# Optimization experiments

Hardware: AMD Instinct MI355X
Metric: run time of the kernel (lower is better)

## Reference

```python
import jax, jax.numpy as jnp
import numpy as np

B, P, L = 1024, 8, 16384  # batch, PRECISION_BITS, TRNG_BITSTREAM_LENGTH


def setup_inputs() -> dict:
    key = jax.random.key(0)
    k1, k2 = jax.random.split(key)
    num = jax.random.randint(k1, (B,), 0, 2 ** P, dtype=jnp.int32)
    # per-module TRNG bitstreams, length P + L (as in Module.__init__)
    r = jax.random.randint(k2, (B, P, P + L), 0, 2, dtype=jnp.int32)
    return {"num": num, "r": r}


def reference(num, r):
    # Module index i reads x[P-1-i] of the MSB-first binary string -> bit i (LSB-first)
    Bsz, Pb, T = r.shape
    Lb = T - Pb
    x = ((num[:, None] >> jnp.arange(Pb, dtype=num.dtype)) & 1).astype(r.dtype)  # [B,P]
    rt = jnp.moveaxis(r, -1, 0)  # [T,B,P]

    def step(y, r_c):
        # majority scheme: y_o = x&y | x&r | y&r  (vectorized over batch and modules)
        y_o = (x & y) | (x & r_c) | (y & r_c)
        # pipeline: y_i[i, t+1] = y_o[i-1, t]; module 0 keeps y_i = 0 forever
        y_next = jnp.concatenate([jnp.zeros((Bsz, 1), r.dtype), y_o[:, :-1]], axis=1)
        return y_next, y_o[:, -1]  # snarf last module's output

    _, outs = jax.lax.scan(step, jnp.zeros((Bsz, Pb), r.dtype), rt)  # outs: [T,B]
    # sn[cyc] = y_o[P-1] from cycle cyc-1; first P entries are invalid and trimmed
    sn = outs[Pb - 1 : Pb - 1 + Lb].T  # [B, L]
    return sn
```

## Files before the change

### kernel.cpp

```cpp
#include <hip/hip_runtime.h>


#define BATCH 1024
#define PBITS 8
#define LBITS 16384
#define TLEN (PBITS + LBITS)

#define CHUNK 4096
#define STAGE_DW 4104

typedef const __attribute__((address_space(1))) void gvoid;
typedef __attribute__((address_space(3))) void lvoid;

__global__ __launch_bounds__(256) void sng_kernel(const int* __restrict__ num,
                                                  const int* __restrict__ r,
                                                  int* __restrict__ out) {
    __shared__ int lds[STAGE_DW];

    const int t = threadIdx.x;
    const int b = blockIdx.x >> 2;
    const int jb = (blockIdx.x & 3) << 12;

    const int nb = num[b];
    const int* rowbase = r + (size_t)b * (PBITS * TLEN) + jb;

    int v[16];
#pragma unroll
    for (int k = 0; k < 16; ++k) v[k] = 0;

#pragma unroll
    for (int i = 0; i < PBITS; ++i) {
        const int* src = rowbase + i * TLEN;
#pragma unroll
        for (int k = 0; k < 4; ++k)
            __builtin_amdgcn_global_load_lds((gvoid*)(src + 4 * (t + 256 * k)),
                                             (lvoid*)(&lds[4 * (t + 256 * k)]),
                                             16, 0, 0);
        if (t < 2)
            __builtin_amdgcn_global_load_lds((gvoid*)(src + 4 * (1024 + t)),
                                             (lvoid*)(&lds[4 * (1024 + t)]),
                                             16, 0, 0);
        __syncthreads();

        const int* lp = &lds[t + i];
        if ((nb >> i) & 1) {
#pragma unroll
            for (int k = 0; k < 16; ++k) v[k] |= lp[256 * k];
        } else {
#pragma unroll
            for (int k = 0; k < 16; ++k) v[k] &= lp[256 * k];
        }
        __syncthreads();
    }

    int* ob = out + (size_t)b * LBITS + jb + t;
#pragma unroll
    for (int k = 0; k < 16; ++k)
        __builtin_nontemporal_store(v[k], ob + 256 * k);
}

extern "C" void kernel_launch(void* const* d_in, const int* in_sizes, int n_in,
                              void* d_out, int out_size, void* d_ws, size_t ws_size,
                              hipStream_t stream) {
    const int* num = (const int*)d_in[0];
    const int* r   = (const int*)d_in[1];
    int* out = (int*)d_out;

    const int blocks = BATCH * 4;
    sng_kernel<<<blocks, 256, 0, stream>>>(num, r, out);
}
```

Measured before the change: 699.2 us.

## Replace LDS staging with direct vector loads and skip leading zero-bit rows

Removes the LDS staging buffer and its two barriers per bit row. Each thread now owns 16 consecutive outputs, reads a 20-int window with five 16-byte nontemporal loads, and writes its results with vector stores. Rows below the lowest set bit of num are skipped, since AND-ing a zero accumulator leaves it zero. In exchange each thread loads 25% more data per row through overlapping windows, and register pressure rises.

```diff
diff --git a/kernel.cpp b/kernel.cpp
--- a/kernel.cpp
+++ b/kernel.cpp
@@ -6,23 +6,20 @@
 #define LBITS 16384
 #define TLEN (PBITS + LBITS)
 
-#define CHUNK 4096
-#define STAGE_DW 4104
-
-typedef const __attribute__((address_space(1))) void gvoid;
-typedef __attribute__((address_space(3))) void lvoid;
+typedef int v4i __attribute__((ext_vector_type(4)));
 
 __global__ __launch_bounds__(256) void sng_kernel(const int* __restrict__ num,
                                                   const int* __restrict__ r,
                                                   int* __restrict__ out) {
-    __shared__ int lds[STAGE_DW];
-
     const int t = threadIdx.x;
     const int b = blockIdx.x >> 2;
     const int jb = (blockIdx.x & 3) << 12;
+    const int l = jb + (t << 4);
 
     const int nb = num[b];
-    const int* rowbase = r + (size_t)b * (PBITS * TLEN) + jb;
+    const int start = __builtin_ctz(nb | (1 << PBITS));
+
+    const int* rb = r + (size_t)b * (PBITS * TLEN) + l;
 
     int v[16];
 #pragma unroll
@@ -30,33 +27,34 @@
 
 #pragma unroll
     for (int i = 0; i < PBITS; ++i) {
-        const int* src = rowbase + i * TLEN;
+        if (i < start) continue;
+        const int* p = rb + (size_t)i * TLEN + 4 * (i >> 2);
+        int a[20];
 #pragma unroll
-        for (int k = 0; k < 4; ++k)
-            __builtin_amdgcn_global_load_lds((gvoid*)(src + 4 * (t + 256 * k)),
-                                             (lvoid*)(&lds[4 * (t + 256 * k)]),
-                                             16, 0, 0);
-        if (t < 2)
-            __builtin_amdgcn_global_load_lds((gvoid*)(src + 4 * (1024 + t)),
-                                             (lvoid*)(&lds[4 * (1024 + t)]),
-                                             16, 0, 0);
-        __syncthreads();
-
-        const int* lp = &lds[t + i];
+        for (int q = 0; q < 5; ++q) {
+            const v4i w = __builtin_nontemporal_load(
+                reinterpret_cast<const v4i*>(p + 4 * q));
+            a[4 * q + 0] = w.x; a[4 * q + 1] = w.y;
+            a[4 * q + 2] = w.z; a[4 * q + 3] = w.w;
+        }
+        const int s = i & 3;
         if ((nb >> i) & 1) {
 #pragma unroll
-            for (int k = 0; k < 16; ++k) v[k] |= lp[256 * k];
+            for (int k = 0; k < 16; ++k) v[k] |= a[s + k];
         } else {
 #pragma unroll
-            for (int k = 0; k < 16; ++k) v[k] &= lp[256 * k];
+            for (int k = 0; k < 16; ++k) v[k] &= a[s + k];
         }
-        __syncthreads();
     }
 
-    int* ob = out + (size_t)b * LBITS + jb + t;
+    int* o = out + (size_t)b * LBITS + l;
 #pragma unroll
-    for (int k = 0; k < 16; ++k)
-        __builtin_nontemporal_store(v[k], ob + 256 * k);
+    for (int q = 0; q < 4; ++q) {
+        v4i w;
+        w.x = v[4 * q + 0]; w.y = v[4 * q + 1];
+        w.z = v[4 * q + 2]; w.w = v[4 * q + 3];
+        __builtin_nontemporal_store(w, reinterpret_cast<v4i*>(o + 4 * q));
+    }
 }
 
 extern "C" void kernel_launch(void* const* d_in, const int* in_sizes, int n_in,
```

New measurement: 754.3 us. 7.9% more time.

## Issue all row loads up front, skip rows below lowest set bit

Applied to the files above, without the earlier changes.

Each block now handles a 1024-element chunk instead of 4096, giving four times as many blocks. It issues the global-to-LDS loads for all needed rows at once into six separate LDS buffers, with a single barrier instead of two barriers per row. Rows 0 and 4 are aligned, so they are loaded straight into registers with nontemporal loads. Rows below the lowest set bit of num are skipped, because an AND into an all-zero accumulator leaves it zero. The aim is more memory parallelism and fewer serialized load/sync phases, at the cost of more LDS per block and more blocks.

```diff
diff --git a/kernel.cpp b/kernel.cpp
--- a/kernel.cpp
+++ b/kernel.cpp
@@ -6,57 +6,82 @@
 #define LBITS 16384
 #define TLEN (PBITS + LBITS)
 
-#define CHUNK 4096
-#define STAGE_DW 4104
-
 typedef const __attribute__((address_space(1))) void gvoid;
 typedef __attribute__((address_space(3))) void lvoid;
 
-__global__ __launch_bounds__(256) void sng_kernel(const int* __restrict__ num,
-                                                  const int* __restrict__ r,
-                                                  int* __restrict__ out) {
-    __shared__ int lds[STAGE_DW];
+__global__ __launch_bounds__(256, 4) void sng_kernel(const int* __restrict__ num,
+                                                     const int* __restrict__ r,
+                                                     int* __restrict__ out) {
+    __shared__ int lds[6][1032];
 
     const int t = threadIdx.x;
-    const int b = blockIdx.x >> 2;
-    const int jb = (blockIdx.x & 3) << 12;
+    const int b = blockIdx.x >> 4;
+    const int jb = (blockIdx.x & 15) << 10;
 
     const int nb = num[b];
-    const int* rowbase = r + (size_t)b * (PBITS * TLEN) + jb;
+    const int start = __builtin_ctz(nb | 256);
 
-    int v[16];
-#pragma unroll
-    for (int k = 0; k < 16; ++k) v[k] = 0;
+    const int* rb = r + (size_t)b * (PBITS * TLEN) + jb;
 
 #pragma unroll
     for (int i = 0; i < PBITS; ++i) {
-        const int* src = rowbase + i * TLEN;
+        if ((i & 3) == 0) continue;
+        if (i >= start) {
+            const int si = (i < 4) ? (i - 1) : (i - 2);
+            const int* src = rb + (size_t)i * TLEN;
+            __builtin_amdgcn_global_load_lds((gvoid*)(src + 4 * t),
+                                             (lvoid*)(&lds[si][4 * t]), 16, 0, 0);
+            if (t < 2)
+                __builtin_amdgcn_global_load_lds((gvoid*)(src + 1024 + 4 * t),
+                                                 (lvoid*)(&lds[si][1024 + 4 * t]),
+                                                 16, 0, 0);
+        }
+    }
+
+    int d0[4], d4[4];
+    if (start == 0) {
 #pragma unroll
         for (int k = 0; k < 4; ++k)
-            __builtin_amdgcn_global_load_lds((gvoid*)(src + 4 * (t + 256 * k)),
-                                             (lvoid*)(&lds[4 * (t + 256 * k)]),
-                                             16, 0, 0);
-        if (t < 2)
-            __builtin_amdgcn_global_load_lds((gvoid*)(src + 4 * (1024 + t)),
-                                             (lvoid*)(&lds[4 * (1024 + t)]),
-                                             16, 0, 0);
-        __syncthreads();
+            d0[k] = __builtin_nontemporal_load(rb + t + 256 * k);
+    }
+    if (start <= 4) {
+#pragma unroll
+        for (int k = 0; k < 4; ++k)
+            d4[k] = __builtin_nontemporal_load(rb + (size_t)4 * TLEN + 4 + t + 256 * k);
+    }
 
-        const int* lp = &lds[t + i];
+    __syncthreads();
+
+    int v[4] = {0, 0, 0, 0};
+#pragma unroll
+    for (int i = 0; i < PBITS; ++i) {
+        if (i < start) continue;
+        int a[4];
+        if (i == 0) {
+#pragma unroll
+            for (int k = 0; k < 4; ++k) a[k] = d0[k];
+        } else if (i == 4) {
+#pragma unroll
+            for (int k = 0; k < 4; ++k) a[k] = d4[k];
+        } else {
+            const int si = (i < 4) ? (i - 1) : (i - 2);
+#pragma unroll
+            for (int k = 0; k < 4; ++k)
+                a[k] = lds[si][t + i + 256 * k];
+        }
         if ((nb >> i) & 1) {
 #pragma unroll
-            for (int k = 0; k < 16; ++k) v[k] |= lp[256 * k];
+            for (int k = 0; k < 4; ++k) v[k] |= a[k];
         } else {
 #pragma unroll
-            for (int k = 0; k < 16; ++k) v[k] &= lp[256 * k];
+            for (int k = 0; k < 4; ++k) v[k] &= a[k];
         }
-        __syncthreads();
     }
 
-    int* ob = out + (size_t)b * LBITS + jb + t;
+    int* o = out + (size_t)b * LBITS + jb + t;
 #pragma unroll
-    for (int k = 0; k < 16; ++k)
-        __builtin_nontemporal_store(v[k], ob + 256 * k);
+    for (int k = 0; k < 4; ++k)
+        __builtin_nontemporal_store(v[k], o + 256 * k);
 }
 
 extern "C" void kernel_launch(void* const* d_in, const int* in_sizes, int n_in,
@@ -66,6 +91,6 @@
     const int* r   = (const int*)d_in[1];
     int* out = (int*)d_out;
 
-    const int blocks = BATCH * 4;
+    const int blocks = BATCH * 16;
     sng_kernel<<<blocks, 256, 0, stream>>>(num, r, out);
 }
```

Result: faster. 684.7 us (-2.1%).
